# Kernel tuning notes

Hardware: AMD Instinct MI355X
Metric: run time of the kernel (lower is better)

The kernel has to match this reference:

```python
import jax, jax.numpy as jnp
import numpy as np

NUM_ITEMS = 10000
EMB_DIM = 32
HIST_LEN = 4_000_000


def setup_inputs() -> dict:
    key = jax.random.key(0)
    k_hist, k_emb = jax.random.split(key)
    user_history = jax.random.randint(k_hist, (HIST_LEN,), 0, NUM_ITEMS, dtype=jnp.int64 if jax.config.jax_enable_x64 else jnp.int32)
    item_embeddings = jax.random.uniform(k_emb, (NUM_ITEMS, EMB_DIM), dtype=jnp.float32)
    return {"user_history": user_history, "item_embeddings": item_embeddings, "k": 10}


def reference(user_history, item_embeddings, k):
    # gather [H, 32] then mean-pool over the history dim -> [32]
    user_embedding = item_embeddings[user_history].mean(axis=0)
    # score every item: [32] @ [32, N] -> [N]
    scores = user_embedding @ item_embeddings.T
    # top-k indices, descending by score (matches torch.topk default)
    _, indices = jax.lax.top_k(scores, k)
    return indices
```

## Files before the change

### kernel.cpp

```cpp
#include <hip/hip_runtime.h>
#include <stdint.h>

#define NITEMS 10000
#define EDIM 32
#define NWORDS 5000

constexpr int NBH = 256;
constexpr int TBH = 1024;
constexpr int NBE = 40;
constexpr int TBE = 1024;
constexpr int WPB = NWORDS / NBE;
constexpr int IPEB = 2 * WPB;
constexpr int CHUNKS = 8;
constexpr int RPC = NBH / CHUNKS;
constexpr int NBS = 40;
constexpr int TBS = 256;
constexpr int IPB = (NITEMS + NBS - 1) / NBS;



__global__ __launch_bounds__(TBH) void k1_hist(
    const int* __restrict__ hist, int H,
    uint32_t* __restrict__ hist_g,
    unsigned int* __restrict__ counter)
{
    __shared__ uint32_t cnt[NWORDS];
    for (int i = threadIdx.x; i < NWORDS; i += TBH) cnt[i] = 0;
    if (blockIdx.x == 0 && threadIdx.x == 0) *counter = 0;
    __syncthreads();

    int tid = blockIdx.x * TBH + threadIdx.x;
    int nth = gridDim.x * TBH;
    const int4* h4 = (const int4*)hist;
    int H4 = H >> 2;
    for (int i = tid; i < H4; i += nth) {
        int4 v = h4[i];
        atomicAdd(&cnt[v.x >> 1], 1u << ((v.x & 1) << 4));
        atomicAdd(&cnt[v.y >> 1], 1u << ((v.y & 1) << 4));
        atomicAdd(&cnt[v.z >> 1], 1u << ((v.z & 1) << 4));
        atomicAdd(&cnt[v.w >> 1], 1u << ((v.w & 1) << 4));
    }
    for (int i = (H4 << 2) + tid; i < H; i += nth) {
        int v = hist[i];
        atomicAdd(&cnt[v >> 1], 1u << ((v & 1) << 4));
    }
    __syncthreads();

    uint32_t* dst = hist_g + (size_t)blockIdx.x * NWORDS;
    for (int i = threadIdx.x; i < NWORDS; i += TBH) dst[i] = cnt[i];
}

__global__ __launch_bounds__(TBE) void k2_merge_embsum(
    const uint32_t* __restrict__ hist_g,
    const float* __restrict__ emb,
    double* __restrict__ partials)
{
    __shared__ uint32_t partLo[CHUNKS][WPB + 3];
    __shared__ uint32_t partHi[CHUNKS][WPB + 3];
    __shared__ int cnt[IPEB];
    __shared__ double sred[TBE / 32][32];

    int t = threadIdx.x;
    int w_idx = t & 127;
    int chunk = t >> 7;
    int wbase = blockIdx.x * WPB;

    if (w_idx < WPB) {
        uint32_t lo = 0, hi = 0;
        const uint32_t* src = hist_g + (size_t)(chunk * RPC) * NWORDS + wbase + w_idx;
        #pragma unroll 8
        for (int r = 0; r < RPC; ++r) {
            uint32_t v = src[(size_t)r * NWORDS];
            lo += v & 0xFFFFu;
            hi += v >> 16;
        }
        partLo[chunk][w_idx] = lo;
        partHi[chunk][w_idx] = hi;
    }
    __syncthreads();

    if (t < WPB) {
        uint32_t lo = 0, hi = 0;
        #pragma unroll
        for (int c = 0; c < CHUNKS; ++c) {
            lo += partLo[c][t];
            hi += partHi[c][t];
        }
        cnt[2 * t]     = (int)lo;
        cnt[2 * t + 1] = (int)hi;
    }
    __syncthreads();

    int d = t & 31;
    int g = t >> 5;
    int ibase = blockIdx.x * IPEB;
    double acc = 0.0;
    for (int i = g; i < IPEB; i += TBE / 32) {
        acc += (double)cnt[i] * (double)emb[(ibase + i) * EDIM + d];
    }
    sred[g][d] = acc;
    __syncthreads();
    if (t < 32) {
        double s = sred[0][t];
        #pragma unroll
        for (int g2 = 1; g2 < TBE / 32; ++g2) s += sred[g2][t];
        partials[blockIdx.x * 32 + t] = s;
    }
}


__global__ __launch_bounds__(1024) void k1_fb_hist_embsum(
    const int* __restrict__ hist, int H,
    const float* __restrict__ emb,
    double* __restrict__ partials)
{
    __shared__ int cnt[NITEMS];
    __shared__ double sred[32][32];

    for (int i = threadIdx.x; i < NITEMS; i += 1024) cnt[i] = 0;
    __syncthreads();

    int tid = blockIdx.x * 1024 + threadIdx.x;
    int nth = gridDim.x * 1024;
    const int4* h4 = (const int4*)hist;
    int H4 = H >> 2;
    for (int i = tid; i < H4; i += nth) {
        int4 v = h4[i];
        atomicAdd(&cnt[v.x], 1);
        atomicAdd(&cnt[v.y], 1);
        atomicAdd(&cnt[v.z], 1);
        atomicAdd(&cnt[v.w], 1);
    }
    for (int i = (H4 << 2) + tid; i < H; i += nth) atomicAdd(&cnt[hist[i]], 1);
    __syncthreads();

    int d = threadIdx.x & 31;
    int g = threadIdx.x >> 5;
    double acc = 0.0;
    for (int i = g; i < NITEMS; i += 32)
        acc += (double)cnt[i] * (double)emb[i * EDIM + d];
    sred[g][d] = acc;
    __syncthreads();
    if (threadIdx.x < 32) {
        double s = 0.0;
        #pragma unroll
        for (int g2 = 0; g2 < 32; ++g2) s += sred[g2][threadIdx.x];
        partials[blockIdx.x * 32 + threadIdx.x] = s;
    }
}


__device__ __forceinline__ unsigned long long umax64(unsigned long long a, unsigned long long b) {
    return a > b ? a : b;
}

__device__ __forceinline__ unsigned long long wave_max64(unsigned long long v) {
    #pragma unroll
    for (int off = 32; off > 0; off >>= 1)
        v = umax64(v, __shfl_xor(v, off));
    return v;
}

__global__ __launch_bounds__(TBS) void k3_score_topk(
    const double* __restrict__ partials, int nparts,
    const float* __restrict__ emb,
    double invH,
    unsigned long long* __restrict__ cand,
    unsigned int* __restrict__ counter,
    int* __restrict__ out, int K)
{
    __shared__ double sred[TBS / 32][32];
    __shared__ float um[EDIM];
    __shared__ unsigned long long wred[TBS / 64];
    __shared__ unsigned long long winner;
    __shared__ int lastFlag;

    int t = threadIdx.x;
    int lane = t & 63;
    int wv = t >> 6;
    constexpr int NW = TBS / 64;

    {
        int d = t & 31;
        int g = t >> 5;
        double acc = 0.0;
        for (int b = g; b < nparts; b += TBS / 32)
            acc += partials[b * EDIM + d];
        sred[g][d] = acc;
        __syncthreads();
        if (t < 32) {
            double s = sred[0][t];
            #pragma unroll
            for (int g2 = 1; g2 < TBS / 32; ++g2) s += sred[g2][t];
            um[t] = (float)(s * invH);
        }
        __syncthreads();
    }

    int item = blockIdx.x * IPB + t;
    unsigned long long my = 0ull;
    if (t < IPB && item < NITEMS) {
        const float4* row = (const float4*)(emb + (size_t)item * EDIM);
        float sc = 0.f;
        #pragma unroll
        for (int q = 0; q < EDIM / 4; ++q) {
            float4 v = row[q];
            sc += um[q * 4 + 0] * v.x + um[q * 4 + 1] * v.y
                + um[q * 4 + 2] * v.z + um[q * 4 + 3] * v.w;
        }
        unsigned int sb = __float_as_uint(sc);
        my = ((unsigned long long)sb << 32)
           | (unsigned long long)(0xFFFFFFFFu - (unsigned int)item);
    }

    for (int it = 0; it < K; ++it) {
        unsigned long long w = wave_max64(my);
        if (lane == 0) wred[wv] = w;
        __syncthreads();
        if (t == 0) {
            unsigned long long win = wred[0];
            #pragma unroll
            for (int j = 1; j < NW; ++j) win = umax64(win, wred[j]);
            winner = win;
            __hip_atomic_store(&cand[blockIdx.x * K + it], win,
                               __ATOMIC_RELAXED, __HIP_MEMORY_SCOPE_AGENT);
        }
        __syncthreads();
        if (my == winner) my = 0ull;
    }

    if (t == 0) {
        unsigned int prev = __hip_atomic_fetch_add(counter, 1u,
                               __ATOMIC_ACQ_REL, __HIP_MEMORY_SCOPE_AGENT);
        lastFlag = (prev == (unsigned int)(gridDim.x - 1));
    }
    __syncthreads();
    if (!lastFlag) return;

    int NC = gridDim.x * K;
    unsigned long long a = 0ull, b = 0ull;
    if (t < NC)
        a = __hip_atomic_load(&cand[t], __ATOMIC_RELAXED, __HIP_MEMORY_SCOPE_AGENT);
    if (t + TBS < NC)
        b = __hip_atomic_load(&cand[t + TBS], __ATOMIC_RELAXED, __HIP_MEMORY_SCOPE_AGENT);

    for (int it = 0; it < K; ++it) {
        unsigned long long m = umax64(a, b);
        unsigned long long w = wave_max64(m);
        if (lane == 0) wred[wv] = w;
        __syncthreads();
        if (t == 0) {
            unsigned long long win = wred[0];
            #pragma unroll
            for (int j = 1; j < NW; ++j) win = umax64(win, wred[j]);
            winner = win;
            out[it] = (int)(0xFFFFFFFFu - (unsigned int)(win & 0xFFFFFFFFull));
        }
        __syncthreads();
        unsigned long long win = winner;
        if (a == win) a = 0ull;
        if (b == win) b = 0ull;
    }
}

extern "C" void kernel_launch(void* const* d_in, const int* in_sizes, int n_in,
                              void* d_out, int out_size, void* d_ws, size_t ws_size,
                              hipStream_t stream) {
    const int*   hist = (const int*)d_in[0];
    const float* emb  = (const float*)d_in[1];
    int H = in_sizes[0];
    int K = out_size;
    double invH = 1.0 / (double)H;
    char* ws = (char*)d_ws;

    constexpr size_t FAST_WS = 5133696;

    if (ws_size >= FAST_WS) {
        uint32_t* hist_g         = (uint32_t*)ws;
        double* partials         = (double*)(ws + 5120000);
        unsigned int* counter    = (unsigned int*)(ws + 5130240);
        unsigned long long* cand = (unsigned long long*)(ws + 5130496);

        hipLaunchKernelGGL(k1_hist, dim3(NBH), dim3(TBH), 0, stream,
                           hist, H, hist_g, counter);
        hipLaunchKernelGGL(k2_merge_embsum, dim3(NBE), dim3(TBE), 0, stream,
                           hist_g, emb, partials);
        hipLaunchKernelGGL(k3_score_topk, dim3(NBS), dim3(TBS), 0, stream,
                           partials, NBE, emb, invH, cand, counter, (int*)d_out, K);
    } else {
        double* partials         = (double*)ws;
        unsigned int* counter    = (unsigned int*)(ws + 65536);
        unsigned long long* cand = (unsigned long long*)(ws + 65792);

        hipMemsetAsync(counter, 0, sizeof(unsigned int), stream);
        hipLaunchKernelGGL(k1_fb_hist_embsum, dim3(256), dim3(1024), 0, stream,
                           hist, H, emb, partials);
        hipLaunchKernelGGL(k3_score_topk, dim3(NBS), dim3(TBS), 0, stream,
                           partials, 256, emb, invH, cand, counter, (int*)d_out, K);
    }
}
```

Baseline: 29.12 us.

## Use per-wave top-k with single-wave merge and unroll histogram loads

After: 31.79 us. 1.09x slower.

```diff
diff --git a/kernel.cpp b/kernel.cpp
--- a/kernel.cpp
+++ b/kernel.cpp
@@ -18,37 +18,58 @@
 constexpr int IPB = (NITEMS + NBS - 1) / NBS;
 
 
+__device__ __forceinline__ unsigned long long umax64(unsigned long long a, unsigned long long b) {
+    return a > b ? a : b;
+}
+__device__ __forceinline__ unsigned long long wave_max64(unsigned long long v) {
+    #pragma unroll
+    for (int off = 32; off > 0; off >>= 1)
+        v = umax64(v, __shfl_xor(v, off));
+    return v;
+}
+
+#define HATOM(v) atomicAdd(&cnt[(v) >> 1], 1u << (((v) & 1) << 4))
+
 
 __global__ __launch_bounds__(TBH) void k1_hist(
     const int* __restrict__ hist, int H,
     uint32_t* __restrict__ hist_g,
-    unsigned int* __restrict__ counter)
+    unsigned int* __restrict__ bar)
 {
     __shared__ uint32_t cnt[NWORDS];
     for (int i = threadIdx.x; i < NWORDS; i += TBH) cnt[i] = 0;
-    if (blockIdx.x == 0 && threadIdx.x == 0) *counter = 0;
+    if (blockIdx.x == 0 && threadIdx.x < 2)
+        __hip_atomic_store(&bar[threadIdx.x], 0u, __ATOMIC_RELAXED, __HIP_MEMORY_SCOPE_AGENT);
     __syncthreads();
 
     int tid = blockIdx.x * TBH + threadIdx.x;
     int nth = gridDim.x * TBH;
     const int4* h4 = (const int4*)hist;
     int H4 = H >> 2;
-    for (int i = tid; i < H4; i += nth) {
-        int4 v = h4[i];
-        atomicAdd(&cnt[v.x >> 1], 1u << ((v.x & 1) << 4));
-        atomicAdd(&cnt[v.y >> 1], 1u << ((v.y & 1) << 4));
-        atomicAdd(&cnt[v.z >> 1], 1u << ((v.z & 1) << 4));
-        atomicAdd(&cnt[v.w >> 1], 1u << ((v.w & 1) << 4));
+
+    for (int base = tid; base < H4; base += 4 * nth) {
+        int i1 = base + nth, i2 = base + 2 * nth, i3 = base + 3 * nth;
+        bool v1 = i1 < H4, v2 = i2 < H4, v3 = i3 < H4;
+        int4 a = h4[base];
+        int4 b, c, d;
+        if (v1) b = h4[i1];
+        if (v2) c = h4[i2];
+        if (v3) d = h4[i3];
+        HATOM(a.x); HATOM(a.y); HATOM(a.z); HATOM(a.w);
+        if (v1) { HATOM(b.x); HATOM(b.y); HATOM(b.z); HATOM(b.w); }
+        if (v2) { HATOM(c.x); HATOM(c.y); HATOM(c.z); HATOM(c.w); }
+        if (v3) { HATOM(d.x); HATOM(d.y); HATOM(d.z); HATOM(d.w); }
     }
     for (int i = (H4 << 2) + tid; i < H; i += nth) {
         int v = hist[i];
-        atomicAdd(&cnt[v >> 1], 1u << ((v & 1) << 4));
+        HATOM(v);
     }
     __syncthreads();
 
     uint32_t* dst = hist_g + (size_t)blockIdx.x * NWORDS;
     for (int i = threadIdx.x; i < NWORDS; i += TBH) dst[i] = cnt[i];
 }
+
 
 __global__ __launch_bounds__(TBE) void k2_merge_embsum(
     const uint32_t* __restrict__ hist_g,
@@ -82,10 +103,7 @@
     if (t < WPB) {
         uint32_t lo = 0, hi = 0;
         #pragma unroll
-        for (int c = 0; c < CHUNKS; ++c) {
-            lo += partLo[c][t];
-            hi += partHi[c][t];
-        }
+        for (int c = 0; c < CHUNKS; ++c) { lo += partLo[c][t]; hi += partHi[c][t]; }
         cnt[2 * t]     = (int)lo;
         cnt[2 * t + 1] = (int)hi;
     }
@@ -95,9 +113,8 @@
     int g = t >> 5;
     int ibase = blockIdx.x * IPEB;
     double acc = 0.0;
-    for (int i = g; i < IPEB; i += TBE / 32) {
+    for (int i = g; i < IPEB; i += TBE / 32)
         acc += (double)cnt[i] * (double)emb[(ibase + i) * EDIM + d];
-    }
     sred[g][d] = acc;
     __syncthreads();
     if (t < 32) {
@@ -150,17 +167,6 @@
 }
 
 
-__device__ __forceinline__ unsigned long long umax64(unsigned long long a, unsigned long long b) {
-    return a > b ? a : b;
-}
-
-__device__ __forceinline__ unsigned long long wave_max64(unsigned long long v) {
-    #pragma unroll
-    for (int off = 32; off > 0; off >>= 1)
-        v = umax64(v, __shfl_xor(v, off));
-    return v;
-}
-
 __global__ __launch_bounds__(TBS) void k3_score_topk(
     const double* __restrict__ partials, int nparts,
     const float* __restrict__ emb,
@@ -171,8 +177,7 @@
 {
     __shared__ double sred[TBS / 32][32];
     __shared__ float um[EDIM];
-    __shared__ unsigned long long wred[TBS / 64];
-    __shared__ unsigned long long winner;
+    __shared__ unsigned long long wlds[(TBS / 64) * 16];
     __shared__ int lastFlag;
 
     int t = threadIdx.x;
@@ -213,25 +218,28 @@
            | (unsigned long long)(0xFFFFFFFFu - (unsigned int)item);
     }
 
-    for (int it = 0; it < K; ++it) {
-        unsigned long long w = wave_max64(my);
-        if (lane == 0) wred[wv] = w;
-        __syncthreads();
-        if (t == 0) {
-            unsigned long long win = wred[0];
-            #pragma unroll
-            for (int j = 1; j < NW; ++j) win = umax64(win, wred[j]);
-            winner = win;
-            __hip_atomic_store(&cand[blockIdx.x * K + it], win,
-                               __ATOMIC_RELAXED, __HIP_MEMORY_SCOPE_AGENT);
-        }
-        __syncthreads();
-        if (my == winner) my = 0ull;
-    }
+    for (int j = 0; j < K; ++j) {
+        unsigned long long win = wave_max64(my);
+        if (lane == 0) wlds[wv * K + j] = win;
+        if (my == win) my = 0ull;
+    }
+    __syncthreads();
+    if (wv == 0) {
+        int NE = NW * K;
+        unsigned long long s = (lane < NE) ? wlds[lane] : 0ull;
+        for (int j = 0; j < K; ++j) {
+            unsigned long long win = wave_max64(s);
+            if (lane == 0)
+                __hip_atomic_store(&cand[blockIdx.x * K + j], win,
+                                   __ATOMIC_RELAXED, __HIP_MEMORY_SCOPE_AGENT);
+            if (s == win) s = 0ull;
+        }
+    }
+    __syncthreads();
 
     if (t == 0) {
         unsigned int prev = __hip_atomic_fetch_add(counter, 1u,
-                               __ATOMIC_ACQ_REL, __HIP_MEMORY_SCOPE_AGENT);
+                               __ATOMIC_RELAXED, __HIP_MEMORY_SCOPE_AGENT);
         lastFlag = (prev == (unsigned int)(gridDim.x - 1));
     }
     __syncthreads();
@@ -244,22 +252,22 @@
     if (t + TBS < NC)
         b = __hip_atomic_load(&cand[t + TBS], __ATOMIC_RELAXED, __HIP_MEMORY_SCOPE_AGENT);
 
-    for (int it = 0; it < K; ++it) {
+    for (int j = 0; j < K; ++j) {
         unsigned long long m = umax64(a, b);
-        unsigned long long w = wave_max64(m);
-        if (lane == 0) wred[wv] = w;
-        __syncthreads();
-        if (t == 0) {
-            unsigned long long win = wred[0];
-            #pragma unroll
-            for (int j = 1; j < NW; ++j) win = umax64(win, wred[j]);
-            winner = win;
-            out[it] = (int)(0xFFFFFFFFu - (unsigned int)(win & 0xFFFFFFFFull));
-        }
-        __syncthreads();
-        unsigned long long win = winner;
+        unsigned long long win = wave_max64(m);
+        if (lane == 0) wlds[wv * K + j] = win;
         if (a == win) a = 0ull;
         if (b == win) b = 0ull;
+    }
+    __syncthreads();
+    if (wv == 0) {
+        int NE = NW * K;
+        unsigned long long s = (lane < NE) ? wlds[lane] : 0ull;
+        for (int j = 0; j < K; ++j) {
+            unsigned long long win = wave_max64(s);
+            if (lane == 0) out[j] = (int)(0xFFFFFFFFu - (unsigned int)(win & 0xFFFFFFFFull));
+            if (s == win) s = 0ull;
+        }
     }
 }
 
@@ -275,18 +283,18 @@
 
     constexpr size_t FAST_WS = 5133696;
 
-    if (ws_size >= FAST_WS) {
+    if (ws_size >= FAST_WS && K <= 16) {
         uint32_t* hist_g         = (uint32_t*)ws;
         double* partials         = (double*)(ws + 5120000);
-        unsigned int* counter    = (unsigned int*)(ws + 5130240);
+        unsigned int* bar        = (unsigned int*)(ws + 5130240);
         unsigned long long* cand = (unsigned long long*)(ws + 5130496);
 
         hipLaunchKernelGGL(k1_hist, dim3(NBH), dim3(TBH), 0, stream,
-                           hist, H, hist_g, counter);
+                           hist, H, hist_g, bar);
         hipLaunchKernelGGL(k2_merge_embsum, dim3(NBE), dim3(TBE), 0, stream,
                            hist_g, emb, partials);
         hipLaunchKernelGGL(k3_score_topk, dim3(NBS), dim3(TBS), 0, stream,
-                           partials, NBE, emb, invH, cand, counter, (int*)d_out, K);
+                           partials, NBE, emb, invH, cand, &bar[1], (int*)d_out, K);
     } else {
         double* partials         = (double*)ws;
         unsigned int* counter    = (unsigned int*)(ws + 65536);
```
